# Performance work log

Measured on AMD Instinct MI355X. Metric: run time of the kernel, lower is better.

## Reference

```python
import jax, jax.numpy as jnp
import numpy as np

NQ = 10          # qubits per register
DIM = 2 ** NQ    # 1024 amplitudes
N_CLS = 10       # canonical images (one per class)
N = 16384        # batch of samples
IMG = 28 * 28    # 784 pixels, zero-padded to DIM


def setup_inputs() -> dict:
    key = jax.random.key(0)
    k1, k2, k3 = jax.random.split(key, 3)
    z_re = jax.random.normal(k1, (N, DIM), dtype=jnp.float32)
    z_im = jax.random.normal(k2, (N, DIM), dtype=jnp.float32)
    # inputs are quantum states -> L2-normalize the complex vectors
    nrm = jnp.sqrt(jnp.sum(z_re * z_re + z_im * z_im, axis=1, keepdims=True))
    z_re = z_re / nrm
    z_im = z_im / nrm
    canon = jax.random.uniform(k3, (N_CLS, 1, 28, 28), dtype=jnp.float32)
    return {"z_re": z_re, "z_im": z_im, "canon": canon}


def reference(z_re, z_im, canon):
    # reshape_norm_padding: flatten, zero-pad to 2^nq, L2-normalize (real amplitudes)
    ref = canon.reshape(N_CLS, IMG)
    ref = jnp.pad(ref, ((0, 0), (0, DIM - IMG)))                  # [C, DIM]
    ref = ref / jnp.linalg.norm(ref, axis=1, keepdims=True)
    # Swap test: <Z_anc> = |<val|ref>|^2. ref is real, so with val = z_re + i*z_im:
    #   <val|ref> = (z_re @ ref^T) - i*(z_im @ ref^T)
    s_re = jnp.einsum('nd,cd->nc', z_re, ref)                     # [N, C]
    s_im = jnp.einsum('nd,cd->nc', z_im, ref)                     # [N, C]
    return s_re * s_re + s_im * s_im                              # [N, C] float32
```

## Files before the change

### kernel.cpp

```cpp
#include <hip/hip_runtime.h>

#define DIM    1024
#define DIM4   256
#define N_CLS  10
#define NROWS  16384
#define IMG    784

#define THREADS  256
#define WAVES_PB 4
#define ROWS_PB  16
#define STEPS    16
#define PSTRIDE  21

__global__ void ref_prep_kernel(const float* __restrict__ canon,
                                float* __restrict__ ref) {
  __shared__ float red[256];
  const int c = blockIdx.x;
  const int t = threadIdx.x;
  const float* src = canon + c * IMG;

  float ss = 0.f;
  for (int d = t; d < IMG; d += 256) {
    float v = src[d];
    ss += v * v;
  }
  red[t] = ss;
  __syncthreads();
  for (int s = 128; s > 0; s >>= 1) {
    if (t < s) red[t] += red[t + s];
    __syncthreads();
  }
  const float inv = 1.0f / sqrtf(red[0]);

  for (int d = t; d < DIM; d += 256) {
    ref[c * DIM + d] = (d < IMG) ? src[d] * inv : 0.f;
  }
}

__global__ __launch_bounds__(THREADS, 4) void swaptest_kernel(
    const float* __restrict__ zre, const float* __restrict__ zim,
    const float* __restrict__ ref, float* __restrict__ out) {
  __shared__ float part[WAVES_PB * 64 * PSTRIDE];

  const int tid  = threadIdx.x;
  const int lane = tid & 63;
  const int wv   = tid >> 6;
  const int q    = lane & 3;
  const int rloc = lane >> 2;

  const int row = blockIdx.x * ROWS_PB + rloc;

  const float4* zr4 = (const float4*)zre + (size_t)row * DIM4 + wv * 64 + q;
  const float4* zi4 = (const float4*)zim + (size_t)row * DIM4 + wv * 64 + q;
  const float4* rf4 = (const float4*)ref + wv * 64 + q;

  float accre[N_CLS], accim[N_CLS];
#pragma unroll
  for (int c = 0; c < N_CLS; ++c) {
    accre[c] = 0.f;
    accim[c] = 0.f;
  }

  float4 cre = zr4[0];
  float4 cim = zi4[0];
#pragma unroll
  for (int s = 0; s < STEPS; ++s) {
    float4 nre, nim;
    if (s + 1 < STEPS) {
      nre = zr4[(s + 1) * 4];
      nim = zi4[(s + 1) * 4];
    }
#pragma unroll
    for (int c = 0; c < N_CLS; ++c) {
      const float4 rv = rf4[c * DIM4 + s * 4];
      accre[c] = fmaf(
          cre.w, rv.w,
          fmaf(cre.z, rv.z, fmaf(cre.y, rv.y, fmaf(cre.x, rv.x, accre[c]))));
      accim[c] = fmaf(
          cim.w, rv.w,
          fmaf(cim.z, rv.z, fmaf(cim.y, rv.y, fmaf(cim.x, rv.x, accim[c]))));
    }
    if (s + 1 < STEPS) {
      cre = nre;
      cim = nim;
    }
  }

  {
    float* pp = &part[(wv * 64 + lane) * PSTRIDE];
#pragma unroll
    for (int c = 0; c < N_CLS; ++c) {
      pp[2 * c]     = accre[c];
      pp[2 * c + 1] = accim[c];
    }
  }
  __syncthreads();

  if (tid < ROWS_PB * N_CLS) {
    const int r = tid / N_CLS;
    const int c = tid - r * N_CLS;
    float are = 0.f, aim = 0.f;
#pragma unroll
    for (int w = 0; w < WAVES_PB; ++w) {
#pragma unroll
      for (int qq = 0; qq < 4; ++qq) {
        const float* sp = &part[(w * 64 + 4 * r + qq) * PSTRIDE];
        are += sp[2 * c];
        aim += sp[2 * c + 1];
      }
    }
    out[(size_t)(blockIdx.x * ROWS_PB + r) * N_CLS + c] = are * are + aim * aim;
  }
}

extern "C" void kernel_launch(void* const* d_in, const int* in_sizes, int n_in,
                              void* d_out, int out_size, void* d_ws,
                              size_t ws_size, hipStream_t stream) {
  const float* z_re = (const float*)d_in[0];
  const float* z_im = (const float*)d_in[1];
  const float* canon = (const float*)d_in[2];
  float* out = (float*)d_out;
  float* ref = (float*)d_ws;

  ref_prep_kernel<<<N_CLS, 256, 0, stream>>>(canon, ref);

  const int nblk = NROWS / ROWS_PB;
  swaptest_kernel<<<nblk, THREADS, 0, stream>>>(z_re, z_im, ref, out);
}
```

Baseline: 159.1 us.

## Compute swap-test overlaps with bf16 MFMA instead of scalar FMAs

Replaces the per-lane FP32 FMA dot products with 16x16x32 bf16 MFMA instructions. The reference matrix is padded to 16 classes and pre-converted to bf16, and the z rows are converted to bf16 on the fly. The K dimension is split across two waves and combined through shared memory. This removes the FP32 ALU work and the repeated reference loads from the inner loop, but the input is memory-bound (128 MB read), and bf16 rounding lowers the accuracy of the results.

New measurement: 152.4 us. 1.04x faster.

```diff
diff --git a/kernel.cpp b/kernel.cpp
--- a/kernel.cpp
+++ b/kernel.cpp
@@ -1,115 +1,140 @@
 #include <hip/hip_runtime.h>
 
 #define DIM    1024
-#define DIM4   256
 #define N_CLS  10
+#define NB     16
 #define NROWS  16384
 #define IMG    784
+#define K_HALF 512
+#define CHUNKS 16
 
-#define THREADS  256
-#define WAVES_PB 4
-#define ROWS_PB  16
-#define STEPS    16
-#define PSTRIDE  21
+typedef __attribute__((ext_vector_type(8))) short sh8;
+typedef __attribute__((ext_vector_type(4))) float f4;
+
+__device__ __forceinline__ unsigned f2bf2(float lo, float hi) {
+  unsigned a = __float_as_uint(lo);
+  unsigned b = __float_as_uint(hi);
+  a += 0x7FFFu + ((a >> 16) & 1u);
+  b += 0x7FFFu + ((b >> 16) & 1u);
+  return (a >> 16) | (b & 0xFFFF0000u);
+}
+
+__device__ __forceinline__ unsigned short f2bf(float x) {
+  unsigned a = __float_as_uint(x);
+  a += 0x7FFFu + ((a >> 16) & 1u);
+  return (unsigned short)(a >> 16);
+}
+
+__device__ __forceinline__ sh8 pack8(f4 v0, f4 v1) {
+  union {
+    unsigned u[4];
+    sh8 s;
+  } r;
+  r.u[0] = f2bf2(v0.x, v0.y);
+  r.u[1] = f2bf2(v0.z, v0.w);
+  r.u[2] = f2bf2(v1.x, v1.y);
+  r.u[3] = f2bf2(v1.z, v1.w);
+  return r.s;
+}
 
 __global__ void ref_prep_kernel(const float* __restrict__ canon,
-                                float* __restrict__ ref) {
+                                unsigned short* __restrict__ refb) {
   __shared__ float red[256];
   const int c = blockIdx.x;
   const int t = threadIdx.x;
-  const float* src = canon + c * IMG;
 
-  float ss = 0.f;
-  for (int d = t; d < IMG; d += 256) {
-    float v = src[d];
-    ss += v * v;
+  float inv = 0.f;
+  if (c < N_CLS) {
+    const float* src = canon + c * IMG;
+    float ss = 0.f;
+    for (int d = t; d < IMG; d += 256) {
+      float v = src[d];
+      ss += v * v;
+    }
+    red[t] = ss;
+    __syncthreads();
+    for (int s = 128; s > 0; s >>= 1) {
+      if (t < s) red[t] += red[t + s];
+      __syncthreads();
+    }
+    inv = 1.0f / sqrtf(red[0]);
   }
-  red[t] = ss;
-  __syncthreads();
-  for (int s = 128; s > 0; s >>= 1) {
-    if (t < s) red[t] += red[t + s];
-    __syncthreads();
-  }
-  const float inv = 1.0f / sqrtf(red[0]);
 
   for (int d = t; d < DIM; d += 256) {
-    ref[c * DIM + d] = (d < IMG) ? src[d] * inv : 0.f;
+    float v = (c < N_CLS && d < IMG) ? canon[c * IMG + d] * inv : 0.f;
+    refb[c * DIM + d] = f2bf(v);
   }
 }
 
-__global__ __launch_bounds__(THREADS, 4) void swaptest_kernel(
+__global__ __launch_bounds__(256, 2) void swaptest_kernel(
     const float* __restrict__ zre, const float* __restrict__ zim,
-    const float* __restrict__ ref, float* __restrict__ out) {
-  __shared__ float part[WAVES_PB * 64 * PSTRIDE];
+    const unsigned short* __restrict__ refb, float* __restrict__ out) {
+  __shared__ float part[8][2][64];
 
   const int tid  = threadIdx.x;
   const int lane = tid & 63;
   const int wv   = tid >> 6;
-  const int q    = lane & 3;
-  const int rloc = lane >> 2;
+  const int st   = wv >> 1;
+  const int kh   = wv & 1;
+  const int mrow = lane & 15;
+  const int kq   = lane >> 4;
 
-  const int row = blockIdx.x * ROWS_PB + rloc;
+  const int row   = blockIdx.x * 32 + st * 16 + mrow;
+  const int kbase = kh * K_HALF + kq * 8;
 
-  const float4* zr4 = (const float4*)zre + (size_t)row * DIM4 + wv * 64 + q;
-  const float4* zi4 = (const float4*)zim + (size_t)row * DIM4 + wv * 64 + q;
-  const float4* rf4 = (const float4*)ref + wv * 64 + q;
+  sh8 bfrag[CHUNKS];
+#pragma unroll
+  for (int i = 0; i < CHUNKS; ++i)
+    bfrag[i] = *(const sh8*)&refb[mrow * DIM + kbase + i * 32];
 
-  float accre[N_CLS], accim[N_CLS];
+  const float* pre = zre + (size_t)row * DIM + kbase;
+  const float* pim = zim + (size_t)row * DIM + kbase;
+
+  f4 accre = {0.f, 0.f, 0.f, 0.f};
+  f4 accim = {0.f, 0.f, 0.f, 0.f};
+
+  f4 cre0 = *(const f4*)(pre);
+  f4 cre1 = *(const f4*)(pre + 4);
+  f4 cim0 = *(const f4*)(pim);
+  f4 cim1 = *(const f4*)(pim + 4);
 #pragma unroll
-  for (int c = 0; c < N_CLS; ++c) {
-    accre[c] = 0.f;
-    accim[c] = 0.f;
-  }
-
-  float4 cre = zr4[0];
-  float4 cim = zi4[0];
-#pragma unroll
-  for (int s = 0; s < STEPS; ++s) {
-    float4 nre, nim;
-    if (s + 1 < STEPS) {
-      nre = zr4[(s + 1) * 4];
-      nim = zi4[(s + 1) * 4];
+  for (int i = 0; i < CHUNKS; ++i) {
+    f4 nre0, nre1, nim0, nim1;
+    if (i + 1 < CHUNKS) {
+      nre0 = *(const f4*)(pre + (i + 1) * 32);
+      nre1 = *(const f4*)(pre + (i + 1) * 32 + 4);
+      nim0 = *(const f4*)(pim + (i + 1) * 32);
+      nim1 = *(const f4*)(pim + (i + 1) * 32 + 4);
     }
-#pragma unroll
-    for (int c = 0; c < N_CLS; ++c) {
-      const float4 rv = rf4[c * DIM4 + s * 4];
-      accre[c] = fmaf(
-          cre.w, rv.w,
-          fmaf(cre.z, rv.z, fmaf(cre.y, rv.y, fmaf(cre.x, rv.x, accre[c]))));
-      accim[c] = fmaf(
-          cim.w, rv.w,
-          fmaf(cim.z, rv.z, fmaf(cim.y, rv.y, fmaf(cim.x, rv.x, accim[c]))));
-    }
-    if (s + 1 < STEPS) {
-      cre = nre;
-      cim = nim;
+    const sh8 a_re = pack8(cre0, cre1);
+    const sh8 a_im = pack8(cim0, cim1);
+    accre = __builtin_amdgcn_mfma_f32_16x16x32_bf16(a_re, bfrag[i], accre,
+                                                    0, 0, 0);
+    accim = __builtin_amdgcn_mfma_f32_16x16x32_bf16(a_im, bfrag[i], accim,
+                                                    0, 0, 0);
+    if (i + 1 < CHUNKS) {
+      cre0 = nre0; cre1 = nre1;
+      cim0 = nim0; cim1 = nim1;
     }
   }
 
-  {
-    float* pp = &part[(wv * 64 + lane) * PSTRIDE];
+  if (kh == 1) {
 #pragma unroll
-    for (int c = 0; c < N_CLS; ++c) {
-      pp[2 * c]     = accre[c];
-      pp[2 * c + 1] = accim[c];
+    for (int r = 0; r < 4; ++r) {
+      part[r][st][lane]     = accre[r];
+      part[4 + r][st][lane] = accim[r];
     }
   }
   __syncthreads();
 
-  if (tid < ROWS_PB * N_CLS) {
-    const int r = tid / N_CLS;
-    const int c = tid - r * N_CLS;
-    float are = 0.f, aim = 0.f;
+  if (kh == 0 && mrow < N_CLS) {
+    const int orow0 = blockIdx.x * 32 + st * 16 + kq * 4;
 #pragma unroll
-    for (int w = 0; w < WAVES_PB; ++w) {
-#pragma unroll
-      for (int qq = 0; qq < 4; ++qq) {
-        const float* sp = &part[(w * 64 + 4 * r + qq) * PSTRIDE];
-        are += sp[2 * c];
-        aim += sp[2 * c + 1];
-      }
+    for (int r = 0; r < 4; ++r) {
+      const float re = accre[r] + part[r][st][lane];
+      const float im = accim[r] + part[4 + r][st][lane];
+      out[(size_t)(orow0 + r) * N_CLS + mrow] = re * re + im * im;
     }
-    out[(size_t)(blockIdx.x * ROWS_PB + r) * N_CLS + c] = are * are + aim * aim;
   }
 }
 
@@ -120,10 +145,10 @@
   const float* z_im = (const float*)d_in[1];
   const float* canon = (const float*)d_in[2];
   float* out = (float*)d_out;
-  float* ref = (float*)d_ws;
+  unsigned short* refb = (unsigned short*)d_ws;
 
-  ref_prep_kernel<<<N_CLS, 256, 0, stream>>>(canon, ref);
+  ref_prep_kernel<<<NB, 256, 0, stream>>>(canon, refb);
 
-  const int nblk = NROWS / ROWS_PB;
-  swaptest_kernel<<<nblk, THREADS, 0, stream>>>(z_re, z_im, ref, out);
+  const int nblk = NROWS / 32;
+  swaptest_kernel<<<nblk, 256, 0, stream>>>(z_re, z_im, refb, out);
 }
```
